# Performance work log

Hardware: AMD Instinct MI355X
Metric: run time of the kernel (lower is better)

Reference implementation:

```python
import jax, jax.numpy as jnp
import numpy as np

N, K = 262144, 8
IN_F, H_F, OUT_F = 16, 128, 16
NEG_SLOPE = 0.01  # torch LeakyReLU default


def setup_inputs() -> dict:
    key = jax.random.key(0)
    ks = jax.random.split(key, 10)
    h = jax.random.normal(ks[0], (N, IN_F), dtype=jnp.float32)
    pos = jax.random.uniform(ks[1], (N, 3), dtype=jnp.float32)
    nbr_idx = jax.random.randint(ks[2], (N, K), 0, N)

    def xavier(k, shape):
        fan_in, fan_out = shape[0], shape[1]
        a = jnp.sqrt(6.0 / (fan_in + fan_out))
        return jax.random.uniform(k, shape, jnp.float32, -a, a)

    W0 = xavier(ks[3], (K * IN_F, H_F))
    b0 = xavier(ks[4], (1, H_F))
    W1 = xavier(ks[5], (K * H_F, H_F))
    b1 = xavier(ks[6], (1, H_F))
    W2 = xavier(ks[7], (K * H_F, OUT_F))
    b2 = xavier(ks[8], (1, OUT_F))
    return {"h": h, "pos": pos, "nbr_idx": nbr_idx,
            "W0": W0, "b0": b0, "W1": W1, "b1": b1, "W2": W2, "b2": b2}


def _layer(h, pos, nbr_idx, W, b, activation):
    # gather neighbor messages and positions: [N, K, F], [N, K, 3]
    msgs = h[nbr_idx]
    src_pos = pos[nbr_idx]
    diff = pos[:, None, :] - src_pos                       # [N, K, 3]
    dist = jnp.sqrt(jnp.sum(diff * diff, axis=2, keepdims=True))  # [N, K, 1]
    dist = jnp.where(dist == 0, jnp.float32(0.5), dist)
    wow = (msgs / dist).reshape(h.shape[0], -1)            # [N, K*F]
    out = wow @ W + b
    if activation:
        out = jnp.where(out >= 0, out, NEG_SLOPE * out)
    return out


def reference(h, pos, nbr_idx, W0, b0, W1, b1, W2, b2):
    h1 = _layer(h, pos, nbr_idx, W0, b0, False)   # input layer
    h2 = _layer(h1, pos, nbr_idx, W1, b1, True)   # hidden layer (LeakyReLU)
    h3 = _layer(h2, pos, nbr_idx, W2, b2, False)  # output layer
    return h3
```

## Files before the change

kernel.cpp:

```cpp
#include <hip/hip_runtime.h>
#include <hip/hip_fp16.h>


typedef _Float16 f16x8 __attribute__((ext_vector_type(8)));
typedef float f32x4 __attribute__((ext_vector_type(4)));

#define NNODES 262144

__global__ __launch_bounds__(256) void prep_all_kernel(
    const float* __restrict__ h, __half* __restrict__ h16,
    const float* __restrict__ pos, const int* __restrict__ nbr,
    __half* __restrict__ invd,
    const float* __restrict__ W0, __half* __restrict__ W0f,
    const float* __restrict__ W1, __half* __restrict__ W1f,
    const float* __restrict__ W2, __half* __restrict__ W2f) {
    const int b = blockIdx.x;
    const int t = threadIdx.x;
    if (b < 16384) {
        int i = b * 256 + t;
        h16[i] = __float2half(h[i]);
    } else if (b < 24576) {
        int e = (b - 16384) * 256 + t;
        int i = e >> 3;
        int n = nbr[e];
        float dx = pos[i * 3 + 0] - pos[n * 3 + 0];
        float dy = pos[i * 3 + 1] - pos[n * 3 + 1];
        float dz = pos[i * 3 + 2] - pos[n * 3 + 2];
        float d = sqrtf(dx * dx + dy * dy + dz * dz);
        if (d == 0.0f) d = 0.5f;
        invd[e] = __float2half((1.0f / d) * 0.00390625f);
    } else if (b < 24640) {
        int e = (b - 24576) * 256 + t;
        int j = e & 7;
        int lane = (e >> 3) & 63;
        int rest = e >> 9;
        int tt = rest % 8;
        int s = rest / 8;
        int k = s * 32 + (lane >> 4) * 8 + j;
        int n = tt * 16 + (lane & 15);
        W0f[e] = __float2half(W0[k * 128 + n]);
    } else if (b < 25152) {
        int e = (b - 24640) * 256 + t;
        int j = e & 7;
        int lane = (e >> 3) & 63;
        int rest = e >> 9;
        int tt = rest % 8;
        int s = rest / 8;
        int k = s * 32 + (lane >> 4) * 8 + j;
        int n = tt * 16 + (lane & 15);
        W1f[e] = __float2half(W1[k * 128 + n]);
    } else {
        int e = (b - 25152) * 256 + t;
        int j = e & 7;
        int lane = (e >> 3) & 63;
        int rest = e >> 9;
        int tt = rest % 8;
        int s = rest / 8;
        int k = s * 32 + (lane >> 4) * 8 + j;
        W2f[e] = __float2half(W2[(size_t)(tt * 128 + k) * 16 + (lane & 15)]);
    }
}

__global__ __launch_bounds__(256) void layer0_kernel(
    const __half* __restrict__ hprev, const __half* __restrict__ invd,
    const int* __restrict__ nbr, const __half* __restrict__ Wf,
    const float* __restrict__ bias, __half* __restrict__ outp) {
    __shared__ __align__(16) __half Bs[16384];

    const int tid = threadIdx.x;
    const int wave = tid >> 6;
    const int lane = tid & 63;
    const int quad = lane >> 4;
    const int lmod = lane & 15;
    const int mbase = blockIdx.x * 128 + wave * 16 + lmod;

    int idx[2][8];
    f16x8 invr[2];
#pragma unroll
    for (int mt = 0; mt < 2; ++mt) {
        const int m = mbase + mt * 64;
        const int4* nrow = (const int4*)(nbr + (size_t)m * 8);
        const int4 iA = nrow[0];
        const int4 iB = nrow[1];
        idx[mt][0] = iA.x; idx[mt][1] = iA.y; idx[mt][2] = iA.z; idx[mt][3] = iA.w;
        idx[mt][4] = iB.x; idx[mt][5] = iB.y; idx[mt][6] = iB.z; idx[mt][7] = iB.w;
        invr[mt] = *(const f16x8*)(invd + (size_t)m * 8);
    }

    f32x4 acc[2][8];
#pragma unroll
    for (int mt = 0; mt < 2; ++mt)
#pragma unroll
        for (int t = 0; t < 8; ++t) acc[mt][t] = f32x4{0.f, 0.f, 0.f, 0.f};

    {
        const uint4* src = (const uint4*)Wf;
        uint4* dst = (uint4*)Bs;
#pragma unroll
        for (int i = 0; i < 8; ++i) dst[i * 256 + tid] = src[i * 256 + tid];
    }
    __syncthreads();

#pragma unroll
    for (int s = 0; s < 4; ++s) {
        const int nb = 2 * s + (quad >> 1);
        f16x8 as[2];
#pragma unroll
        for (int mt = 0; mt < 2; ++mt) {
            f16x8 av = *(const f16x8*)(hprev + (size_t)idx[mt][nb] * 16 + (quad & 1) * 8);
            as[mt] = av * invr[mt][nb];
        }
#pragma unroll
        for (int t = 0; t < 8; ++t) {
            f16x8 b = *(const f16x8*)(Bs + ((size_t)(s * 8 + t) * 64 + lane) * 8);
#pragma unroll
            for (int mt = 0; mt < 2; ++mt)
                acc[mt][t] = __builtin_amdgcn_mfma_f32_16x16x32_f16(as[mt], b, acc[mt][t], 0, 0, 0);
        }
    }

    __syncthreads();
#pragma unroll
    for (int mt = 0; mt < 2; ++mt) {
#pragma unroll
        for (int t = 0; t < 8; ++t) {
            const int col = t * 16 + lmod;
            const float bv = bias[col];
#pragma unroll
            for (int rr = 0; rr < 4; ++rr) {
                const int lrow = mt * 64 + wave * 16 + quad * 4 + rr;
                float v = acc[mt][t][rr] * 256.0f + bv;
                Bs[lrow * 128 + col] = __float2half(v);
            }
        }
    }
    __syncthreads();
    {
        const int lrow = tid >> 1;
        const int cb = (tid & 1) * 64;
        __half* gdst = outp + (size_t)(blockIdx.x * 128 + lrow) * 128 + cb;
        const __half* lsrc = Bs + lrow * 128 + cb;
#pragma unroll
        for (int j = 0; j < 8; ++j)
            *(f16x8*)(gdst + j * 8) = *(const f16x8*)(lsrc + j * 8);
    }
}

__device__ __forceinline__ int off16(int seg, int row) {
    return seg * 64 + (row & ~15) + ((row ^ seg) & 15);
}

__global__ __launch_bounds__(512, 4) void layer1p_kernel(
    const __half* __restrict__ hprev, const __half* __restrict__ invd,
    const int* __restrict__ nbr, const __half* __restrict__ Wf,
    const __half* __restrict__ Wf2s, const float* __restrict__ bias,
    __half* __restrict__ Pout) {
    __shared__ __align__(16) __half As[2][8192];

    const int tid = threadIdx.x;
    const int wave = tid >> 6;
    const int lane = tid & 63;
    const int quad = lane >> 4;
    const int lmod = lane & 15;
    const int rowblk = blockIdx.x * 64;
    const int seg = lmod;

    const int r0 = wave * 4 + quad;
    const int* nbp = nbr + (size_t)(rowblk + r0) * 8;
    const __half* ivp = invd + (size_t)(rowblk + r0) * 8;

    const int soff0 = off16(seg, r0) * 8;
    const int soff1 = off16(seg, r0 + 32) * 8;

    int roff4[4];
#pragma unroll
    for (int ks = 0; ks < 4; ++ks) {
        const int sg = ks * 4 + quad;
        roff4[ks] = (sg * 64 + ((lmod ^ sg) & 15)) * 8;
    }

    const __half* WfB = Wf + ((size_t)wave * 64 + lane) * 8;

    f16x8 Bc[2], Bn[2];
#pragma unroll
    for (int ks2 = 0; ks2 < 2; ++ks2)
        Bc[ks2] = *(const f16x8*)(WfB + (size_t)ks2 * 4096);

    f16x8 ga[2][2];
    {
        int id0[2], id1[2];
        id0[0] = nbp[0];   id0[1] = nbp[256];
        ga[0][0] = *(const f16x8*)(hprev + (size_t)id0[0] * 128 + seg * 8);
        ga[0][1] = *(const f16x8*)(hprev + (size_t)id0[1] * 128 + seg * 8);
        id1[0] = nbp[1];   id1[1] = nbp[257];
        ga[1][0] = *(const f16x8*)(hprev + (size_t)id1[0] * 128 + seg * 8);
        ga[1][1] = *(const f16x8*)(hprev + (size_t)id1[1] * 128 + seg * 8);
    }

    {
        const _Float16 s0 = *(const _Float16*)(ivp + 0);
        const _Float16 s1 = *(const _Float16*)(ivp + 256);
        *(f16x8*)(&As[0][soff0]) = ga[0][0] * s0;
        *(f16x8*)(&As[0][soff1]) = ga[0][1] * s1;
    }
    __syncthreads();

    f32x4 acc[4];
#pragma unroll
    for (int m = 0; m < 4; ++m) acc[m] = f32x4{0.f, 0.f, 0.f, 0.f};

#pragma unroll
    for (int nb = 0; nb < 8; ++nb) {
        const int cur = nb & 1;
        if (nb < 6) {
            int idn[2];
            idn[0] = nbp[nb + 2];
            idn[1] = nbp[nb + 258];
            ga[cur][0] = *(const f16x8*)(hprev + (size_t)idn[0] * 128 + seg * 8);
            ga[cur][1] = *(const f16x8*)(hprev + (size_t)idn[1] * 128 + seg * 8);
        }
#pragma unroll
        for (int h = 0; h < 2; ++h) {
            const int p = nb * 2 + h;
            if (p < 15) {
#pragma unroll
                for (int ks2 = 0; ks2 < 2; ++ks2)
                    Bn[ks2] = *(const f16x8*)(WfB + (size_t)((p + 1) * 2 + ks2) * 4096);
            }
#pragma unroll
            for (int m = 0; m < 4; ++m) {
#pragma unroll
                for (int ks2 = 0; ks2 < 2; ++ks2) {
                    f16x8 a = *(const f16x8*)(&As[cur][roff4[h * 2 + ks2] + m * 128]);
                    acc[m] = __builtin_amdgcn_mfma_f32_16x16x32_f16(a, Bc[ks2], acc[m], 0, 0, 0);
                }
            }
            Bc[0] = Bn[0];
            Bc[1] = Bn[1];
        }
        if (nb < 7) {
            const _Float16 s0 = *(const _Float16*)(ivp + nb + 1);
            const _Float16 s1 = *(const _Float16*)(ivp + nb + 257);
            *(f16x8*)(&As[cur ^ 1][soff0]) = ga[(nb + 1) & 1][0] * s0;
            *(f16x8*)(&As[cur ^ 1][soff1]) = ga[(nb + 1) & 1][1] * s1;
            __syncthreads();
        }
    }

    __half* As0 = &As[0][0];
    {
        const int col = wave * 16 + lmod;
        const float bv = bias[col];
        const int sg = col >> 3;
        const int jj = col & 7;
#pragma unroll
        for (int m = 0; m < 4; ++m) {
#pragma unroll
            for (int rr = 0; rr < 4; ++rr) {
                const int row = m * 16 + quad * 4 + rr;
                float v = acc[m][rr] * 256.0f + bv;
                v = (v >= 0.f) ? v : 0.01f * v;
                As0[off16(sg, row) * 8 + jj] = __float2half(v);
            }
        }
    }
    __syncthreads();

    const __half* WfB2 = Wf2s + ((size_t)wave * 64 + lane) * 8;
    f16x8 B2[4];
#pragma unroll
    for (int ks = 0; ks < 4; ++ks)
        B2[ks] = *(const f16x8*)(WfB2 + (size_t)ks * 4096);

    f32x4 acc2[4];
#pragma unroll
    for (int m = 0; m < 4; ++m) acc2[m] = f32x4{0.f, 0.f, 0.f, 0.f};
#pragma unroll
    for (int m = 0; m < 4; ++m) {
#pragma unroll
        for (int ks = 0; ks < 4; ++ks) {
            f16x8 a2 = *(const f16x8*)(&As0[roff4[ks] + m * 128]);
            acc2[m] = __builtin_amdgcn_mfma_f32_16x16x32_f16(a2, B2[ks], acc2[m], 0, 0, 0);
        }
    }

    {
        const int col = wave * 16 + lmod;
#pragma unroll
        for (int m = 0; m < 4; ++m) {
#pragma unroll
            for (int rr = 0; rr < 4; ++rr) {
                const int grow = rowblk + m * 16 + quad * 4 + rr;
                Pout[(size_t)grow * 128 + col] = __float2half(acc2[m][rr]);
            }
        }
    }
}

__global__ __launch_bounds__(256) void reduce_kernel(
    const __half* __restrict__ P, const __half* __restrict__ invd,
    const int* __restrict__ nbr, const float* __restrict__ b2,
    float* __restrict__ outp) {
    const int t = blockIdx.x * 256 + threadIdx.x;
    const int d = t >> 1;
    const int half = t & 1;

    const int4* nrow = (const int4*)(nbr + (size_t)d * 8);
    const int4 iA = nrow[0];
    const int4 iB = nrow[1];
    const int idx[8] = {iA.x, iA.y, iA.z, iA.w, iB.x, iB.y, iB.z, iB.w};
    const f16x8 iv = *(const f16x8*)(invd + (size_t)d * 8);

    f16x8 v[8];
#pragma unroll
    for (int k = 0; k < 8; ++k)
        v[k] = *(const f16x8*)(P + (size_t)idx[k] * 128 + k * 16 + half * 8);

    float acc[8];
#pragma unroll
    for (int c = 0; c < 8; ++c) acc[c] = 0.f;
#pragma unroll
    for (int k = 0; k < 8; ++k) {
        const float w = (float)iv[k];
#pragma unroll
        for (int c = 0; c < 8; ++c) acc[c] += w * (float)v[k][c];
    }

    const float* bp = b2 + half * 8;
    float4 o[2];
#pragma unroll
    for (int q = 0; q < 2; ++q) {
        o[q].x = acc[q * 4 + 0] * 256.0f + bp[q * 4 + 0];
        o[q].y = acc[q * 4 + 1] * 256.0f + bp[q * 4 + 1];
        o[q].z = acc[q * 4 + 2] * 256.0f + bp[q * 4 + 2];
        o[q].w = acc[q * 4 + 3] * 256.0f + bp[q * 4 + 3];
    }
    float4* dst = (float4*)(outp + (size_t)d * 16 + half * 8);
    dst[0] = o[0];
    dst[1] = o[1];
}

extern "C" void kernel_launch(void* const* d_in, const int* in_sizes, int n_in,
                              void* d_out, int out_size, void* d_ws, size_t ws_size,
                              hipStream_t stream) {
    const float* h   = (const float*)d_in[0];
    const float* pos = (const float*)d_in[1];
    const int*   nbr = (const int*)d_in[2];
    const float* W0  = (const float*)d_in[3];
    const float* b0  = (const float*)d_in[4];
    const float* W1  = (const float*)d_in[5];
    const float* b1  = (const float*)d_in[6];
    const float* W2  = (const float*)d_in[7];
    const float* b2  = (const float*)d_in[8];

    const int N = NNODES;

    char* w = (char*)d_ws;
    __half* h1 = (__half*)w;
    __half* P  = (__half*)(w + (size_t)67108864);
    __half* invd2 = (__half*)w;

    char* ob = (char*)d_out;
    __half* invd = (__half*)(ob + 0);
    __half* h16  = (__half*)(ob + 4194304);
    __half* W0f  = (__half*)(ob + 12582912);
    __half* W1f  = (__half*)(ob + 12615680);
    __half* Wf2s = (__half*)(ob + 12877824);

    prep_all_kernel<<<25216, 256, 0, stream>>>(h, h16, pos, nbr, invd,
                                               W0, W0f, W1, W1f, W2, Wf2s);

    layer0_kernel<<<N / 128, 256, 0, stream>>>(h16, invd, nbr, W0f, b0, h1);
    layer1p_kernel<<<N / 64, 512, 0, stream>>>(h1, invd, nbr, W1f, Wf2s, b1, P);

    (void)hipMemcpyAsync(invd2, invd, 4194304, hipMemcpyDeviceToDevice, stream);

    reduce_kernel<<<(N * 2) / 256, 256, 0, stream>>>(P, invd2, nbr, b2, (float*)d_out);
}
```

Measured before the change: 313.7 us.

## Fuse h fp16 conversion and inverse-distance computation into layer0 kernel

Moves the float-to-half conversion of h and the per-edge inverse distance computation out of the prep kernel and into layer0, which now gathers fp32 h directly and computes 1/d from pos in registers. Layer0 writes invd for later layers. This removes a large elementwise pass and its global memory round trip, and shrinks the prep kernel to weight repacking. The cost is that layer0 gathers twice as many bytes per neighbor row in fp32 and does extra pos gathers and sqrt work. The weight-to-LDS copy is also moved earlier so it can overlap with the index loads.

```diff
diff --git a/kernel.cpp b/kernel.cpp
--- a/kernel.cpp
+++ b/kernel.cpp
@@ -8,29 +8,13 @@
 #define NNODES 262144
 
 __global__ __launch_bounds__(256) void prep_all_kernel(
-    const float* __restrict__ h, __half* __restrict__ h16,
-    const float* __restrict__ pos, const int* __restrict__ nbr,
-    __half* __restrict__ invd,
     const float* __restrict__ W0, __half* __restrict__ W0f,
     const float* __restrict__ W1, __half* __restrict__ W1f,
     const float* __restrict__ W2, __half* __restrict__ W2f) {
     const int b = blockIdx.x;
     const int t = threadIdx.x;
-    if (b < 16384) {
-        int i = b * 256 + t;
-        h16[i] = __float2half(h[i]);
-    } else if (b < 24576) {
-        int e = (b - 16384) * 256 + t;
-        int i = e >> 3;
-        int n = nbr[e];
-        float dx = pos[i * 3 + 0] - pos[n * 3 + 0];
-        float dy = pos[i * 3 + 1] - pos[n * 3 + 1];
-        float dz = pos[i * 3 + 2] - pos[n * 3 + 2];
-        float d = sqrtf(dx * dx + dy * dy + dz * dz);
-        if (d == 0.0f) d = 0.5f;
-        invd[e] = __float2half((1.0f / d) * 0.00390625f);
-    } else if (b < 24640) {
-        int e = (b - 24576) * 256 + t;
+    if (b < 64) {
+        int e = b * 256 + t;
         int j = e & 7;
         int lane = (e >> 3) & 63;
         int rest = e >> 9;
@@ -39,8 +23,8 @@
         int k = s * 32 + (lane >> 4) * 8 + j;
         int n = tt * 16 + (lane & 15);
         W0f[e] = __float2half(W0[k * 128 + n]);
-    } else if (b < 25152) {
-        int e = (b - 24640) * 256 + t;
+    } else if (b < 576) {
+        int e = (b - 64) * 256 + t;
         int j = e & 7;
         int lane = (e >> 3) & 63;
         int rest = e >> 9;
@@ -50,7 +34,7 @@
         int n = tt * 16 + (lane & 15);
         W1f[e] = __float2half(W1[k * 128 + n]);
     } else {
-        int e = (b - 25152) * 256 + t;
+        int e = (b - 576) * 256 + t;
         int j = e & 7;
         int lane = (e >> 3) & 63;
         int rest = e >> 9;
@@ -62,9 +46,10 @@
 }
 
 __global__ __launch_bounds__(256) void layer0_kernel(
-    const __half* __restrict__ hprev, const __half* __restrict__ invd,
+    const float* __restrict__ h, const float* __restrict__ pos,
     const int* __restrict__ nbr, const __half* __restrict__ Wf,
-    const float* __restrict__ bias, __half* __restrict__ outp) {
+    const float* __restrict__ bias, __half* __restrict__ invd,
+    __half* __restrict__ outp) {
     __shared__ __align__(16) __half Bs[16384];
 
     const int tid = threadIdx.x;
@@ -74,8 +59,14 @@
     const int lmod = lane & 15;
     const int mbase = blockIdx.x * 128 + wave * 16 + lmod;
 
+    {
+        const uint4* src = (const uint4*)Wf;
+        uint4* dst = (uint4*)Bs;
+#pragma unroll
+        for (int i = 0; i < 8; ++i) dst[i * 256 + tid] = src[i * 256 + tid];
+    }
+
     int idx[2][8];
-    f16x8 invr[2];
 #pragma unroll
     for (int mt = 0; mt < 2; ++mt) {
         const int m = mbase + mt * 64;
@@ -84,7 +75,26 @@
         const int4 iB = nrow[1];
         idx[mt][0] = iA.x; idx[mt][1] = iA.y; idx[mt][2] = iA.z; idx[mt][3] = iA.w;
         idx[mt][4] = iB.x; idx[mt][5] = iB.y; idx[mt][6] = iB.z; idx[mt][7] = iB.w;
-        invr[mt] = *(const f16x8*)(invd + (size_t)m * 8);
+    }
+
+    f16x8 invr[2];
+#pragma unroll
+    for (int mt = 0; mt < 2; ++mt) {
+        const int m = mbase + mt * 64;
+        const float px = pos[m * 3 + 0];
+        const float py = pos[m * 3 + 1];
+        const float pz = pos[m * 3 + 2];
+#pragma unroll
+        for (int k = 0; k < 8; ++k) {
+            const int n = idx[mt][k];
+            const float dx = px - pos[n * 3 + 0];
+            const float dy = py - pos[n * 3 + 1];
+            const float dz = pz - pos[n * 3 + 2];
+            float d = sqrtf(dx * dx + dy * dy + dz * dz);
+            if (d == 0.0f) d = 0.5f;
+            invr[mt][k] = (_Float16)((1.0f / d) * 0.00390625f);
+        }
+        if (quad == 0) *(f16x8*)(invd + (size_t)m * 8) = invr[mt];
     }
 
     f32x4 acc[2][8];
@@ -93,12 +103,6 @@
 #pragma unroll
         for (int t = 0; t < 8; ++t) acc[mt][t] = f32x4{0.f, 0.f, 0.f, 0.f};
 
-    {
-        const uint4* src = (const uint4*)Wf;
-        uint4* dst = (uint4*)Bs;
-#pragma unroll
-        for (int i = 0; i < 8; ++i) dst[i * 256 + tid] = src[i * 256 + tid];
-    }
     __syncthreads();
 
 #pragma unroll
@@ -107,7 +111,14 @@
         f16x8 as[2];
 #pragma unroll
         for (int mt = 0; mt < 2; ++mt) {
-            f16x8 av = *(const f16x8*)(hprev + (size_t)idx[mt][nb] * 16 + (quad & 1) * 8);
+            const float* hp = h + (size_t)idx[mt][nb] * 16 + (quad & 1) * 8;
+            const float4 f0 = *(const float4*)(hp);
+            const float4 f1 = *(const float4*)(hp + 4);
+            f16x8 av;
+            av[0] = (_Float16)f0.x; av[1] = (_Float16)f0.y;
+            av[2] = (_Float16)f0.z; av[3] = (_Float16)f0.w;
+            av[4] = (_Float16)f1.x; av[5] = (_Float16)f1.y;
+            av[6] = (_Float16)f1.z; av[7] = (_Float16)f1.w;
             as[mt] = av * invr[mt][nb];
         }
 #pragma unroll
@@ -362,15 +373,13 @@
 
     char* ob = (char*)d_out;
     __half* invd = (__half*)(ob + 0);
-    __half* h16  = (__half*)(ob + 4194304);
-    __half* W0f  = (__half*)(ob + 12582912);
-    __half* W1f  = (__half*)(ob + 12615680);
-    __half* Wf2s = (__half*)(ob + 12877824);
-
-    prep_all_kernel<<<25216, 256, 0, stream>>>(h, h16, pos, nbr, invd,
-                                               W0, W0f, W1, W1f, W2, Wf2s);
-
-    layer0_kernel<<<N / 128, 256, 0, stream>>>(h16, invd, nbr, W0f, b0, h1);
+    __half* W0f  = (__half*)(ob + 4194304);
+    __half* W1f  = (__half*)(ob + 4227072);
+    __half* Wf2s = (__half*)(ob + 4489216);
+
+    prep_all_kernel<<<640, 256, 0, stream>>>(W0, W0f, W1, W1f, W2, Wf2s);
+
+    layer0_kernel<<<N / 128, 256, 0, stream>>>(h, pos, nbr, W0f, b0, invd, h1);
     layer1p_kernel<<<N / 64, 512, 0, stream>>>(h1, invd, nbr, W1f, Wf2s, b1, P);
 
     (void)hipMemcpyAsync(invd2, invd, 4194304, hipMemcpyDeviceToDevice, stream);
```

Result: no change. 313.5 us (-0.0%).
